# Kernel optimization log

Measured on AMD Instinct MI355X. Metric: run time of the kernel, lower is better.

## Reference

```python
import jax, jax.numpy as jnp
import numpy as np

B, L, D, H, NE, M = 4, 1024, 768, 12, 42, 8
OFFSET = 1
NEG = -1e9

def setup_inputs() -> dict:
    key = jax.random.key(0)
    k1, k2, k3, k4 = jax.random.split(key, 4)
    sequence_output = jax.random.normal(k1, (B, L, D), dtype=jnp.float32)
    attention = jax.random.uniform(k2, (B, H, L, L), dtype=jnp.float32)
    mention_idx = jax.random.randint(k3, (B, NE, M), 0, L - 2).astype(jnp.int32)
    mention_mask = jax.random.randint(k4, (B, NE, M), 0, 2).astype(jnp.int32)
    mention_mask = mention_mask.at[:, :, 0].set(1)  # every entity has >=1 mention
    return {"sequence_output": sequence_output, "attention": attention,
            "mention_idx": mention_idx, "mention_mask": mention_mask}

def reference(sequence_output, attention, mention_idx, mention_mask):
    b, l, d = sequence_output.shape
    h = attention.shape[1]
    idx = mention_idx + OFFSET                      # start + offset
    valid = (mention_mask > 0) & (idx < l)          # [B,NE,M], mirrors start+offset < c check
    idx = jnp.where(valid, idx, 0)

    # --- get_hrt: entity embedding = logsumexp over mentions, entity attn = mean over mentions ---
    flat = idx.reshape(b, -1)
    emb = jax.vmap(lambda s, i: s[i])(sequence_output, flat).reshape(b, NE, M, d)
    masked = jnp.where(valid[..., None], emb, NEG)
    ent_emb = jax.nn.logsumexp(masked, axis=2)      # [B,NE,D] (unused downstream, kept faithful)

    att = jax.vmap(lambda a, i: a[:, i])(attention, flat)        # [B,H,NE*M,L]
    att = att.reshape(b, h, NE, M, l)
    vmask = valid.astype(att.dtype)[:, None, :, :, None]         # [B,1,NE,M,1]
    cnt = jnp.maximum(valid.sum(axis=2), 1).astype(att.dtype)    # [B,NE]
    ent_att = (att * vmask).sum(axis=3) / cnt[:, None, :, None]  # [B,H,NE,L]

    # --- get_channel_map: ht_att = mean_h(h_att * t_att), row-normalize, contract with tokens ---
    ht_att = jnp.einsum('bhsl,bhtl->bstl', ent_att, ent_att) / h  # [B,NE,NE,L]
    ht_att = ht_att / (ht_att.sum(axis=-1, keepdims=True) + 1e-5)
    feature_map = jnp.einsum('bstl,bld->bstd', ht_att, sequence_output)  # [B,NE,NE,D]
    return feature_map
```

## Files before the change

kernel.cpp:

```cpp
#include <hip/hip_runtime.h>
#include <math.h>

#define B_    4
#define L_    1024
#define D_    768
#define H_    12
#define NE_   42
#define M_    8
#define NE2_  (NE_ * NE_)
#define NTRI_ 903
#define MPAD_ 1024
#define LC_   16
#define NCH_  (L_ / LC_)

typedef unsigned short u16;
typedef unsigned int   u32;
typedef __attribute__((ext_vector_type(2))) float f32x2;

__device__ __forceinline__ u16 f2bf(float f) {
    union { float f; u32 u; } c; c.f = f;
    u32 u = c.u;
    u32 r = (u + 0x7FFFu + ((u >> 16) & 1u)) >> 16;
    return (u16)r;
}

#define TBLKS (D_/32 * L_/32 * B_)
#define EBLKS (H_ * NE_ * B_)

__global__ __launch_bounds__(256) void prep_kernel(
    const float* __restrict__ S, u16* __restrict__ T,
    const float* __restrict__ att, const int* __restrict__ midx,
    const int* __restrict__ mmask, float* __restrict__ ent) {
    const int bid = blockIdx.x;
    const int tid = threadIdx.x;

    if (bid < TBLKS) {
        __shared__ u16 tile[32][33];
        const int bx = bid % (D_/32);
        const int by = (bid / (D_/32)) % (L_/32);
        const int b  = bid / (D_/32 * L_/32);
        const int n0 = bx * 32, k0 = by * 32;
        const int tx = tid & 31, ty = tid >> 5;
        const float* Sb = S + (size_t)b * L_ * D_;
        u16*         Tb = T + (size_t)b * D_ * L_;
        #pragma unroll
        for (int i = 0; i < 4; ++i)
            tile[ty + i*8][tx] = f2bf(Sb[(size_t)(k0 + ty + i*8) * D_ + (n0 + tx)]);
        __syncthreads();
        #pragma unroll
        for (int i = 0; i < 4; ++i)
            Tb[(size_t)(n0 + ty + i*8) * L_ + (k0 + tx)] = tile[tx][ty + i*8];
    } else {
        const int eb = bid - TBLKS;
        const int h  = eb % H_;
        const int e  = (eb / H_) % NE_;
        const int b  = eb / (H_ * NE_);
        const int l0 = tid * 4;
        const int mb = (b * NE_ + e) * M_;
        const size_t abase = ((size_t)(b * H_ + h)) * L_ * L_;

        float a0 = 0.f, a1 = 0.f, a2 = 0.f, a3 = 0.f;
        int cnt = 0;
        for (int m = 0; m < M_; ++m) {
            int  im = midx[mb + m] + 1;
            bool v  = (mmask[mb + m] > 0) && (im < L_);
            if (v) {
                ++cnt;
                float4 x = *(const float4*)(att + abase + (size_t)im * L_ + l0);
                a0 += x.x; a1 += x.y; a2 += x.z; a3 += x.w;
            }
        }
        const float s = 1.0f / (float)(cnt < 1 ? 1 : cnt);
        float* o = ent + (((size_t)(b * H_ + h)) * NE_ + e) * L_ + l0;
        *(float4*)(o) = make_float4(a0*s, a1*s, a2*s, a3*s);
    }
}

__global__ __launch_bounds__(256) void gram_kernel(
    const float* __restrict__ ent,
    u16* __restrict__ W,
    float* __restrict__ psum)
{
    __shared__ float E[H_ * NE_ * 18 + 8];
    const int gid   = blockIdx.x;
    const int xcd   = gid & 7, rr = gid >> 3;
    const int chunk = xcd * 8 + (rr & 7);
    const int b     = rr >> 3;
    const int l0    = chunk * LC_;
    const int tid   = threadIdx.x;

    const float* Eb = ent + (size_t)b * (H_ * NE_) * L_ + l0;
    for (int i = tid; i < H_ * NE_ * 4; i += 256) {
        const int row = i >> 2, sub = (i & 3) * 4;
        float4 v = *(const float4*)(Eb + (size_t)row * L_ + sub);
        f32x2* d = (f32x2*)&E[row * 18 + sub];
        d[0] = f32x2{v.x, v.y};
        d[1] = f32x2{v.z, v.w};
    }
    __syncthreads();

    if (tid < 231) {
        const int st = tid % 21, tt = tid / 21;
        const int s0 = 2 * st, t0 = 4 * tt;
        if (s0 <= t0 + 3) {
            const int e2 = (t0 + 2 < NE_) ? t0 + 2 : NE_ - 1;
            const int e3 = (t0 + 3 < NE_) ? t0 + 3 : NE_ - 1;
            float ps[2][4] = {};
            for (int l2 = 0; l2 < LC_ / 2; ++l2) {
                const int ll = 2 * l2;
                f32x2 c[2][4] = {};
                #pragma unroll
                for (int h = 0; h < H_; ++h) {
                    const float* Eh = E + h * (NE_ * 18);
                    f32x2 a0 = *(const f32x2*)&Eh[(s0    ) * 18 + ll];
                    f32x2 a1 = *(const f32x2*)&Eh[(s0 + 1) * 18 + ll];
                    f32x2 b0 = *(const f32x2*)&Eh[(t0    ) * 18 + ll];
                    f32x2 b1 = *(const f32x2*)&Eh[(t0 + 1) * 18 + ll];
                    f32x2 b2 = *(const f32x2*)&Eh[(e2    ) * 18 + ll];
                    f32x2 b3 = *(const f32x2*)&Eh[(e3    ) * 18 + ll];
                    c[0][0] += a0 * b0; c[0][1] += a0 * b1;
                    c[0][2] += a0 * b2; c[0][3] += a0 * b3;
                    c[1][0] += a1 * b0; c[1][1] += a1 * b1;
                    c[1][2] += a1 * b2; c[1][3] += a1 * b3;
                }
                #pragma unroll
                for (int si = 0; si < 2; ++si) {
                    #pragma unroll
                    for (int tj = 0; tj < 4; ++tj) {
                        const int s = s0 + si, t = t0 + tj;
                        if (t < NE_ && s <= t) {
                            const int q = (s * (85 - s)) / 2 + (t - s);
                            u32 w = (u32)f2bf(c[si][tj][0]) |
                                    ((u32)f2bf(c[si][tj][1]) << 16);
                            *(u32*)(W + ((size_t)b * MPAD_ + q) * L_ + l0 + ll) = w;
                            ps[si][tj] += c[si][tj][0] + c[si][tj][1];
                        }
                    }
                }
            }
            #pragma unroll
            for (int si = 0; si < 2; ++si)
                #pragma unroll
                for (int tj = 0; tj < 4; ++tj) {
                    const int s = s0 + si, t = t0 + tj;
                    if (t < NE_ && s <= t) {
                        const int q = (s * (85 - s)) / 2 + (t - s);
                        psum[((size_t)b * MPAD_ + q) * NCH_ + chunk] = ps[si][tj];
                    }
                }
        }
    } else {
        for (int q = NTRI_ + (tid - 231); q < MPAD_; q += 25) {
            u16* wr = W + ((size_t)b * MPAD_ + q) * L_ + l0;
            uint4 z; z.x = z.y = z.z = z.w = 0u;
            *(uint4*)(wr)     = z;
            *(uint4*)(wr + 8) = z;
        }
    }
}

typedef __attribute__((ext_vector_type(8))) __bf16 bf16x8;
typedef __attribute__((ext_vector_type(4))) float  f32x4;

__global__ __launch_bounds__(256) void gemm_kernel(
    const u16* __restrict__ W, const u16* __restrict__ T,
    const float* __restrict__ psum, float* __restrict__ out) {
    __shared__ __align__(16) u16 As[2][128 * 64];
    __shared__ __align__(16) u16 Bs[2][128 * 64];
    __shared__ float rs_s[128];
    const int b = blockIdx.z;
    const u16* Ab = W + (size_t)b * MPAD_ * L_ + (size_t)blockIdx.x * 128 * L_;
    const u16* Bb = T + (size_t)b * D_   * L_ + (size_t)blockIdx.y * 128 * L_;
    const int tid  = threadIdx.x;
    const int wave = tid >> 6, lane = tid & 63;
    const int wm = (wave & 1) * 64, wn = (wave >> 1) * 64;
    const int rm = lane & 15, kq = (lane >> 4) * 8;

    auto STAGE = [&](int buf, int k0) {
        #pragma unroll
        for (int i = 0; i < 4; ++i) {
            const int c   = i * 256 + tid;
            const int row = c >> 3, cp = c & 7;
            const int ko  = ((cp ^ (row & 7)) << 3);
            __builtin_amdgcn_global_load_lds(
                (const __attribute__((address_space(1))) void*)(Ab + (size_t)row * L_ + k0 + ko),
                (__attribute__((address_space(3))) void*)(&As[buf][c * 8]), 16, 0, 0);
            __builtin_amdgcn_global_load_lds(
                (const __attribute__((address_space(1))) void*)(Bb + (size_t)row * L_ + k0 + ko),
                (__attribute__((address_space(3))) void*)(&Bs[buf][c * 8]), 16, 0, 0);
        }
    };

    f32x4 acc[4][4] = {};

    STAGE(0, 0);
    if (tid < 128) {
        const float* p = psum + ((size_t)b * MPAD_ + (size_t)blockIdx.x * 128 + tid) * NCH_;
        float s = 0.f;
        #pragma unroll
        for (int i = 0; i < NCH_ / 4; ++i) {
            float4 v = *(const float4*)(p + 4 * i);
            s += v.x + v.y + v.z + v.w;
        }
        rs_s[tid] = 1.0f / (s + (float)H_ * 1e-5f);
    }
    asm volatile("s_waitcnt vmcnt(0) lgkmcnt(0)" ::: "memory");
    __builtin_amdgcn_s_barrier();

    int cur = 0;
    for (int kt = 0; kt < 16; ++kt) {
        if (kt < 15) STAGE(cur ^ 1, (kt + 1) * 64);

        #pragma unroll
        for (int kk = 0; kk < 64; kk += 32) {
            bf16x8 af[4], bfr[4];
            #pragma unroll
            for (int i = 0; i < 4; ++i) {
                const int ra = wm + i*16 + rm;
                af[i]  = *(const bf16x8*)&As[cur][ra * 64 + ((((kk + kq) >> 3) ^ (ra & 7)) << 3)];
            }
            #pragma unroll
            for (int j = 0; j < 4; ++j) {
                const int rb = wn + j*16 + rm;
                bfr[j] = *(const bf16x8*)&Bs[cur][rb * 64 + ((((kk + kq) >> 3) ^ (rb & 7)) << 3)];
            }
            #pragma unroll
            for (int i = 0; i < 4; ++i)
                #pragma unroll
                for (int j = 0; j < 4; ++j)
                    acc[i][j] = __builtin_amdgcn_mfma_f32_16x16x32_bf16(
                                    af[i], bfr[j], acc[i][j], 0, 0, 0);
        }

        asm volatile("s_waitcnt vmcnt(0)" ::: "memory");
        __builtin_amdgcn_s_barrier();
        cur ^= 1;
    }

    const int row0 = blockIdx.x * 128 + wm;
    const int col0 = blockIdx.y * 128 + wn;
    const int cl = lane & 15, rq = (lane >> 4) * 4;
    float* Ob = out + (size_t)b * NE2_ * D_;
    #pragma unroll
    for (int i = 0; i < 4; ++i) {
        #pragma unroll
        for (int r = 0; r < 4; ++r) {
            const int q = row0 + i*16 + rq + r;
            if (q < NTRI_) {
                int s = (int)(42.5f - sqrtf(1806.25f - 2.0f * (float)q));
                if (s < 0) s = 0; if (s > 41) s = 41;
                int base = (s * (85 - s)) >> 1;
                if (q < base) { --s; base = (s * (85 - s)) >> 1; }
                else { const int nb = ((s + 1) * (84 - s)) >> 1;
                       if (q >= nb) { ++s; base = nb; } }
                const int t = s + (q - base);
                const float sc = rs_s[q - blockIdx.x * 128];
                float* O1 = Ob + (size_t)(s * NE_ + t) * D_ + col0 + cl;
                float* O2 = Ob + (size_t)(t * NE_ + s) * D_ + col0 + cl;
                #pragma unroll
                for (int j = 0; j < 4; ++j) {
                    const float v = acc[i][j][r] * sc;
                    O1[j * 16] = v;
                    O2[j * 16] = v;
                }
            }
        }
    }
}

#define ENT_BYTES  (8257536)
#define W_BYTES    (8388608)
#define ST_BYTES   (6291456)

extern "C" void kernel_launch(void* const* d_in, const int* in_sizes, int n_in,
                              void* d_out, int out_size, void* d_ws, size_t ws_size,
                              hipStream_t stream) {
    const float* seq   = (const float*)d_in[0];
    const float* att   = (const float*)d_in[1];
    const int*   midx  = (const int*)d_in[2];
    const int*   mmask = (const int*)d_in[3];
    float* out = (float*)d_out;

    char* ws  = (char*)d_ws;
    float* ent  = (float*)ws;
    u16*   Wb   = (u16*)(ws + ENT_BYTES);
    u16*   ST   = (u16*)(ws + ENT_BYTES + W_BYTES);
    float* psum = (float*)(ws + ENT_BYTES + W_BYTES + ST_BYTES);

    prep_kernel<<<TBLKS + EBLKS, 256, 0, stream>>>(seq, ST, att, midx, mmask, ent);
    gram_kernel<<<256, 256, 0, stream>>>(ent, Wb, psum);
    gemm_kernel<<<dim3(MPAD_/128, D_/128, B_), 256, 0, stream>>>(Wb, ST, psum, out);
}
```

Baseline: 294.1 us.

## Fuse entity-attention gather into gram kernel and drop ent intermediate buffer

Merges the mention-averaging of attention rows into the gram blocks. Each gram block now gathers the attention slices it needs for its L-chunk straight from global memory into shared memory. This removes the write and re-read of the fp32 ent buffer (about 8 MB) and one kernel launch; the transpose blocks now run in the same launch after the gram blocks. The per-call zeroing of the padded W rows beyond the triangle is also removed, so those rows hold whatever is left in the workspace. The gathers are now 64-byte row segments instead of full-row vector loads, which may lower memory efficiency.

After: 316.3 us. +7.6%, slower.

```diff
diff --git a/kernel.cpp b/kernel.cpp
--- a/kernel.cpp
+++ b/kernel.cpp
@@ -24,138 +24,130 @@
     return (u16)r;
 }
 
+#define GBLKS 256
 #define TBLKS (D_/32 * L_/32 * B_)
-#define EBLKS (H_ * NE_ * B_)
-
-__global__ __launch_bounds__(256) void prep_kernel(
+
+__global__ __launch_bounds__(256) void fused_prep_gram(
+    const float* __restrict__ att, const int* __restrict__ midx,
+    const int* __restrict__ mmask,
     const float* __restrict__ S, u16* __restrict__ T,
-    const float* __restrict__ att, const int* __restrict__ midx,
-    const int* __restrict__ mmask, float* __restrict__ ent) {
+    u16* __restrict__ W, float* __restrict__ psum) {
+    __shared__ float E[H_ * NE_ * 18 + 8];
+    __shared__ int   vidx[NE_ * M_];
+    __shared__ float rcp[NE_];
+    __shared__ u16   tile[32][33];
+
     const int bid = blockIdx.x;
     const int tid = threadIdx.x;
 
-    if (bid < TBLKS) {
-        __shared__ u16 tile[32][33];
-        const int bx = bid % (D_/32);
-        const int by = (bid / (D_/32)) % (L_/32);
-        const int b  = bid / (D_/32 * L_/32);
-        const int n0 = bx * 32, k0 = by * 32;
-        const int tx = tid & 31, ty = tid >> 5;
-        const float* Sb = S + (size_t)b * L_ * D_;
-        u16*         Tb = T + (size_t)b * D_ * L_;
-        #pragma unroll
-        for (int i = 0; i < 4; ++i)
-            tile[ty + i*8][tx] = f2bf(Sb[(size_t)(k0 + ty + i*8) * D_ + (n0 + tx)]);
-        __syncthreads();
-        #pragma unroll
-        for (int i = 0; i < 4; ++i)
-            Tb[(size_t)(n0 + ty + i*8) * L_ + (k0 + tx)] = tile[tx][ty + i*8];
-    } else {
-        const int eb = bid - TBLKS;
-        const int h  = eb % H_;
-        const int e  = (eb / H_) % NE_;
-        const int b  = eb / (H_ * NE_);
-        const int l0 = tid * 4;
-        const int mb = (b * NE_ + e) * M_;
-        const size_t abase = ((size_t)(b * H_ + h)) * L_ * L_;
-
-        float a0 = 0.f, a1 = 0.f, a2 = 0.f, a3 = 0.f;
-        int cnt = 0;
-        for (int m = 0; m < M_; ++m) {
-            int  im = midx[mb + m] + 1;
-            bool v  = (mmask[mb + m] > 0) && (im < L_);
-            if (v) {
-                ++cnt;
-                float4 x = *(const float4*)(att + abase + (size_t)im * L_ + l0);
-                a0 += x.x; a1 += x.y; a2 += x.z; a3 += x.w;
-            }
-        }
-        const float s = 1.0f / (float)(cnt < 1 ? 1 : cnt);
-        float* o = ent + (((size_t)(b * H_ + h)) * NE_ + e) * L_ + l0;
-        *(float4*)(o) = make_float4(a0*s, a1*s, a2*s, a3*s);
-    }
-}
-
-__global__ __launch_bounds__(256) void gram_kernel(
-    const float* __restrict__ ent,
-    u16* __restrict__ W,
-    float* __restrict__ psum)
-{
-    __shared__ float E[H_ * NE_ * 18 + 8];
-    const int gid   = blockIdx.x;
-    const int xcd   = gid & 7, rr = gid >> 3;
-    const int chunk = xcd * 8 + (rr & 7);
-    const int b     = rr >> 3;
-    const int l0    = chunk * LC_;
-    const int tid   = threadIdx.x;
-
-    const float* Eb = ent + (size_t)b * (H_ * NE_) * L_ + l0;
-    for (int i = tid; i < H_ * NE_ * 4; i += 256) {
-        const int row = i >> 2, sub = (i & 3) * 4;
-        float4 v = *(const float4*)(Eb + (size_t)row * L_ + sub);
-        f32x2* d = (f32x2*)&E[row * 18 + sub];
-        d[0] = f32x2{v.x, v.y};
-        d[1] = f32x2{v.z, v.w};
-    }
-    __syncthreads();
-
-    if (tid < 231) {
-        const int st = tid % 21, tt = tid / 21;
-        const int s0 = 2 * st, t0 = 4 * tt;
-        if (s0 <= t0 + 3) {
-            const int e2 = (t0 + 2 < NE_) ? t0 + 2 : NE_ - 1;
-            const int e3 = (t0 + 3 < NE_) ? t0 + 3 : NE_ - 1;
-            float ps[2][4] = {};
-            for (int l2 = 0; l2 < LC_ / 2; ++l2) {
-                const int ll = 2 * l2;
-                f32x2 c[2][4] = {};
-                #pragma unroll
-                for (int h = 0; h < H_; ++h) {
-                    const float* Eh = E + h * (NE_ * 18);
-                    f32x2 a0 = *(const f32x2*)&Eh[(s0    ) * 18 + ll];
-                    f32x2 a1 = *(const f32x2*)&Eh[(s0 + 1) * 18 + ll];
-                    f32x2 b0 = *(const f32x2*)&Eh[(t0    ) * 18 + ll];
-                    f32x2 b1 = *(const f32x2*)&Eh[(t0 + 1) * 18 + ll];
-                    f32x2 b2 = *(const f32x2*)&Eh[(e2    ) * 18 + ll];
-                    f32x2 b3 = *(const f32x2*)&Eh[(e3    ) * 18 + ll];
-                    c[0][0] += a0 * b0; c[0][1] += a0 * b1;
-                    c[0][2] += a0 * b2; c[0][3] += a0 * b3;
-                    c[1][0] += a1 * b0; c[1][1] += a1 * b1;
-                    c[1][2] += a1 * b2; c[1][3] += a1 * b3;
+    if (bid < GBLKS) {
+        const int xcd   = bid & 7, rr = bid >> 3;
+        const int chunk = xcd * 8 + (rr & 7);
+        const int b     = rr >> 3;
+        const int l0    = chunk * LC_;
+
+        for (int i = tid; i < NE_ * M_; i += 256) {
+            const int im = midx[b * NE_ * M_ + i] + 1;
+            const bool v = (mmask[b * NE_ * M_ + i] > 0) && (im < L_);
+            vidx[i] = v ? im : -1;
+        }
+        __syncthreads();
+        if (tid < NE_) {
+            int c = 0;
+            #pragma unroll
+            for (int m = 0; m < M_; ++m) c += (vidx[tid * M_ + m] >= 0);
+            rcp[tid] = 1.0f / (float)(c < 1 ? 1 : c);
+        }
+        __syncthreads();
+
+        const float* ab0 = att + (size_t)b * H_ * L_ * L_ + l0;
+        for (int i = tid; i < H_ * NE_ * 4; i += 256) {
+            const int row = i >> 2, sub = (i & 3) * 4;
+            const int h = row / NE_, e = row - h * NE_;
+            const float* ab = ab0 + (size_t)h * L_ * L_ + sub;
+            float a0 = 0.f, a1 = 0.f, a2 = 0.f, a3 = 0.f;
+            #pragma unroll
+            for (int m = 0; m < M_; ++m) {
+                const int im = vidx[e * M_ + m];
+                if (im >= 0) {
+                    float4 x = *(const float4*)(ab + (size_t)im * L_);
+                    a0 += x.x; a1 += x.y; a2 += x.z; a3 += x.w;
+                }
+            }
+            const float s = rcp[e];
+            f32x2* d = (f32x2*)&E[row * 18 + sub];
+            d[0] = f32x2{a0 * s, a1 * s};
+            d[1] = f32x2{a2 * s, a3 * s};
+        }
+        __syncthreads();
+
+        if (tid < 231) {
+            const int st = tid % 21, tt = tid / 21;
+            const int s0 = 2 * st, t0 = 4 * tt;
+            if (s0 <= t0 + 3) {
+                const int e2 = (t0 + 2 < NE_) ? t0 + 2 : NE_ - 1;
+                const int e3 = (t0 + 3 < NE_) ? t0 + 3 : NE_ - 1;
+                float ps[2][4] = {};
+                for (int l2 = 0; l2 < LC_ / 2; ++l2) {
+                    const int ll = 2 * l2;
+                    f32x2 c[2][4] = {};
+                    #pragma unroll
+                    for (int h = 0; h < H_; ++h) {
+                        const float* Eh = E + h * (NE_ * 18);
+                        f32x2 a0 = *(const f32x2*)&Eh[(s0    ) * 18 + ll];
+                        f32x2 a1 = *(const f32x2*)&Eh[(s0 + 1) * 18 + ll];
+                        f32x2 b0 = *(const f32x2*)&Eh[(t0    ) * 18 + ll];
+                        f32x2 b1 = *(const f32x2*)&Eh[(t0 + 1) * 18 + ll];
+                        f32x2 b2 = *(const f32x2*)&Eh[(e2    ) * 18 + ll];
+                        f32x2 b3 = *(const f32x2*)&Eh[(e3    ) * 18 + ll];
+                        c[0][0] += a0 * b0; c[0][1] += a0 * b1;
+                        c[0][2] += a0 * b2; c[0][3] += a0 * b3;
+                        c[1][0] += a1 * b0; c[1][1] += a1 * b1;
+                        c[1][2] += a1 * b2; c[1][3] += a1 * b3;
+                    }
+                    #pragma unroll
+                    for (int si = 0; si < 2; ++si) {
+                        #pragma unroll
+                        for (int tj = 0; tj < 4; ++tj) {
+                            const int s = s0 + si, t = t0 + tj;
+                            if (t < NE_ && s <= t) {
+                                const int q = (s * (85 - s)) / 2 + (t - s);
+                                u32 w = (u32)f2bf(c[si][tj][0]) |
+                                        ((u32)f2bf(c[si][tj][1]) << 16);
+                                *(u32*)(W + ((size_t)b * MPAD_ + q) * L_ + l0 + ll) = w;
+                                ps[si][tj] += c[si][tj][0] + c[si][tj][1];
+                            }
+                        }
+                    }
                 }
                 #pragma unroll
-                for (int si = 0; si < 2; ++si) {
+                for (int si = 0; si < 2; ++si)
                     #pragma unroll
                     for (int tj = 0; tj < 4; ++tj) {
                         const int s = s0 + si, t = t0 + tj;
                         if (t < NE_ && s <= t) {
                             const int q = (s * (85 - s)) / 2 + (t - s);
-                            u32 w = (u32)f2bf(c[si][tj][0]) |
-                                    ((u32)f2bf(c[si][tj][1]) << 16);
-                            *(u32*)(W + ((size_t)b * MPAD_ + q) * L_ + l0 + ll) = w;
-                            ps[si][tj] += c[si][tj][0] + c[si][tj][1];
+                            psum[((size_t)b * MPAD_ + q) * NCH_ + chunk] = ps[si][tj];
                         }
                     }
-                }
-            }
-            #pragma unroll
-            for (int si = 0; si < 2; ++si)
-                #pragma unroll
-                for (int tj = 0; tj < 4; ++tj) {
-                    const int s = s0 + si, t = t0 + tj;
-                    if (t < NE_ && s <= t) {
-                        const int q = (s * (85 - s)) / 2 + (t - s);
-                        psum[((size_t)b * MPAD_ + q) * NCH_ + chunk] = ps[si][tj];
-                    }
-                }
+            }
         }
     } else {
-        for (int q = NTRI_ + (tid - 231); q < MPAD_; q += 25) {
-            u16* wr = W + ((size_t)b * MPAD_ + q) * L_ + l0;
-            uint4 z; z.x = z.y = z.z = z.w = 0u;
-            *(uint4*)(wr)     = z;
-            *(uint4*)(wr + 8) = z;
-        }
+        const int tb = bid - GBLKS;
+        const int bx = tb % (D_/32);
+        const int by = (tb / (D_/32)) % (L_/32);
+        const int b  = tb / (D_/32 * L_/32);
+        const int n0 = bx * 32, k0 = by * 32;
+        const int tx = tid & 31, ty = tid >> 5;
+        const float* Sb = S + (size_t)b * L_ * D_;
+        u16*         Tb = T + (size_t)b * D_ * L_;
+        #pragma unroll
+        for (int i = 0; i < 4; ++i)
+            tile[ty + i*8][tx] = f2bf(Sb[(size_t)(k0 + ty + i*8) * D_ + (n0 + tx)]);
+        __syncthreads();
+        #pragma unroll
+        for (int i = 0; i < 4; ++i)
+            Tb[(size_t)(n0 + ty + i*8) * L_ + (k0 + tx)] = tile[tx][ty + i*8];
     }
 }
 
@@ -268,7 +260,6 @@
     }
 }
 
-#define ENT_BYTES  (8257536)
 #define W_BYTES    (8388608)
 #define ST_BYTES   (6291456)
 
@@ -282,12 +273,11 @@
     float* out = (float*)d_out;
 
     char* ws  = (char*)d_ws;
-    float* ent  = (float*)ws;
-    u16*   Wb   = (u16*)(ws + ENT_BYTES);
-    u16*   ST   = (u16*)(ws + ENT_BYTES + W_BYTES);
-    float* psum = (float*)(ws + ENT_BYTES + W_BYTES + ST_BYTES);
-
-    prep_kernel<<<TBLKS + EBLKS, 256, 0, stream>>>(seq, ST, att, midx, mmask, ent);
-    gram_kernel<<<256, 256, 0, stream>>>(ent, Wb, psum);
+    u16*   Wb   = (u16*)ws;
+    u16*   ST   = (u16*)(ws + W_BYTES);
+    float* psum = (float*)(ws + W_BYTES + ST_BYTES);
+
+    fused_prep_gram<<<GBLKS + TBLKS, 256, 0, stream>>>(att, midx, mmask,
+                                                       seq, ST, Wb, psum);
     gemm_kernel<<<dim3(MPAD_/128, D_/128, B_), 256, 0, stream>>>(Wb, ST, psum, out);
 }
```
